# Kernel optimization log

Measured on AMD Instinct MI355X. Metric: run time of the kernel, lower is better.

The kernel has to match this reference:

```python
import jax, jax.numpy as jnp
import numpy as np

N = 200000   # nodes
E = 600000   # edges (avg degree 3, proof graphs are sparse)
L = 4        # num_layers
ND = 64      # ndim (hardcoded in module)
ED = 12      # edim (hardcoded in module)
V = 80       # len(atom_map)
SCALE = 1.0 / np.sqrt(ND).astype(np.float32)


def setup_inputs() -> dict:
    key = jax.random.key(0)
    ks = jax.random.split(key, 20)
    nrm = lambda k, s: jax.random.normal(k, s, jnp.float32) * 0.05
    return {
        "atoms": jax.random.randint(ks[0], (N,), 0, V),
        "edge_index": jax.random.randint(ks[1], (2, E), 0, N),
        "edge_ids": jax.random.randint(ks[2], (E,), 0, 3),
        "atom_emb": nrm(ks[3], (V, ND)),
        "edge_emb": nrm(ks[4], (3, ED)),
        # dim 0: 0 = r2c convs, 1 = c2r convs; dim 1: layer
        "Wq": nrm(ks[5], (2, L, ND, ND)), "bq": nrm(ks[6], (2, L, ND)),
        "Wk": nrm(ks[7], (2, L, ND, ND)), "bk": nrm(ks[8], (2, L, ND)),
        "Wv": nrm(ks[9], (2, L, ND, ND)), "bv": nrm(ks[10], (2, L, ND)),
        "We": nrm(ks[11], (2, L, ED, ND)),            # lin_edge, bias=False (PyG)
        "Ws": nrm(ks[12], (2, L, ND, ND)), "bs": nrm(ks[13], (2, L, ND)),  # root skip
        "aggr_W": nrm(ks[14], (2 * ND, ND)), "aggr_b": nrm(ks[15], (ND,)),
    }


def tconv(x, src, tgt, e_proj, Wq, bq, Wk, bk, Wv, bv, Ws, bs):
    """PyG TransformerConv (heads=1, concat=True, root_weight=True).
    Messages flow src -> tgt; softmax grouped by tgt."""
    q = x @ Wq + bq                                   # [N, ND]
    k = x @ Wk + bk
    v = x @ Wv + bv
    ke = k[src] + e_proj                              # [E, ND]
    ve = v[src] + e_proj
    alpha = jnp.einsum('ed,ed->e', q[tgt], ke) * SCALE
    amax = jax.ops.segment_max(alpha, tgt, num_segments=N)
    ex = jnp.exp(alpha - amax[tgt])
    den = jax.ops.segment_sum(ex, tgt, num_segments=N)
    w = ex / (den[tgt] + 1e-16)                       # segment softmax
    out = jax.ops.segment_sum(ve * w[:, None], tgt, num_segments=N)
    return out + x @ Ws + bs                          # skip connection


def reference(atoms, edge_index, edge_ids, atom_emb, edge_emb,
              Wq, bq, Wk, bk, Wv, bv, We, Ws, bs, aggr_W, aggr_b):
    # dropout omitted (eval mode / identity)
    x = atom_emb[atoms]                               # [N, ND]
    e = edge_emb[edge_ids]                            # [E, ED]
    src, tgt = edge_index[0], edge_index[1]
    for hop in range(L):
        r2c = tconv(x, src, tgt, e @ We[0, hop],
                    Wq[0, hop], bq[0, hop], Wk[0, hop], bk[0, hop],
                    Wv[0, hop], bv[0, hop], Ws[0, hop], bs[0, hop])
        # edge_index.flip(0): swap src/tgt
        c2r = tconv(x, tgt, src, e @ We[1, hop],
                    Wq[1, hop], bq[1, hop], Wk[1, hop], bk[1, hop],
                    Wv[1, hop], bv[1, hop], Ws[1, hop], bs[1, hop])
        h = jnp.concatenate([r2c, c2r], axis=-1) @ aggr_W + aggr_b
        x = jax.nn.gelu(h, approximate=False)         # torch GELU = exact erf
    return x
```

## Files before the change

kernel.cpp:

```cpp
#include <hip/hip_runtime.h>
#include <hip/hip_bf16.h>

typedef unsigned short u16;
typedef unsigned int u32;
typedef unsigned long long u64;
typedef __attribute__((ext_vector_type(8))) short short8v;
typedef __attribute__((ext_vector_type(4))) float f32x4;

#define SCALE 0.125f

__device__ __forceinline__ float bf2f(u16 u){
    union { u32 i; float f; } c; c.i = ((u32)u) << 16; return c.f;
}
__device__ __forceinline__ u16 f2bf(float f){
    __hip_bfloat16 h = __float2bfloat16(f);
    union { __hip_bfloat16 h; u16 u; } c; c.h = h; return c.u;
}

__global__ void k_gather(const int* __restrict__ atoms, const float* __restrict__ emb,
                         float* __restrict__ x, int n){
    int i = blockIdx.x * blockDim.x + threadIdx.x;
    if (i >= n * 16) return;
    int node = i >> 4, f = i & 15;
    int a = atoms[node];
    ((float4*)x)[i] = ((const float4*)emb)[a * 16 + f];
}

__global__ void k_ew(const float* __restrict__ edge_emb, const float* __restrict__ We,
                     float* __restrict__ EW){
    int t = blockIdx.x * blockDim.x + threadIdx.x;
    if (t >= 2 * 4 * 3 * 64) return;
    int j = t & 63, r = t >> 6;
    int eid = r % 3, dh = r / 3;
    float s = 0.f;
    for (int c = 0; c < 12; ++c)
        s += edge_emb[eid * 12 + c] * We[(dh * 12 + c) * 64 + j];
    EW[(dh * 3 + eid) * 64 + j] = s;
}

__global__ void k_count(const int* __restrict__ ei, u32* cnt_t, u32* cnt_s, int E){
    int e = blockIdx.x * blockDim.x + threadIdx.x;
    if (e >= E) return;
    atomicAdd(&cnt_t[ei[E + e]], 1u);
    atomicAdd(&cnt_s[ei[e]], 1u);
}

__global__ __launch_bounds__(256) void k_scan(
    const u32* __restrict__ cnt_t, const u32* __restrict__ cnt_s,
    u32* __restrict__ start_t, u32* __restrict__ start_s,
    u64* __restrict__ totals, int n)
{
    __shared__ u32 wsum_t[4], wsum_s[4];
    __shared__ u32 base_t, base_s;
    const int t0 = blockIdx.x * 1024 + threadIdx.x * 4;
    u32 ct[4], cs[4];
    #pragma unroll
    for (int j = 0; j < 4; ++j){
        int idx = t0 + j;
        ct[j] = (idx < n) ? cnt_t[idx] : 0u;
        cs[j] = (idx < n) ? cnt_s[idx] : 0u;
    }
    u32 tsum_t = ct[0] + ct[1] + ct[2] + ct[3];
    u32 tsum_s = cs[0] + cs[1] + cs[2] + cs[3];
    const int lane = threadIdx.x & 63, wv = threadIdx.x >> 6;
    u32 it = tsum_t, is = tsum_s;
    for (int d = 1; d < 64; d <<= 1){
        u32 a = __shfl_up(it, d);
        u32 b = __shfl_up(is, d);
        if (lane >= d){ it += a; is += b; }
    }
    if (lane == 63){ wsum_t[wv] = it; wsum_s[wv] = is; }
    __syncthreads();
    if (threadIdx.x == 0){
        u32 a0 = wsum_t[0], a1 = wsum_t[1], a2 = wsum_t[2], a3 = wsum_t[3];
        u32 b0 = wsum_s[0], b1 = wsum_s[1], b2 = wsum_s[2], b3 = wsum_s[3];
        u64 old = atomicAdd(totals, ((u64)(b0 + b1 + b2 + b3) << 32) | (u64)(a0 + a1 + a2 + a3));
        base_t = (u32)(old & 0xFFFFFFFFull);
        base_s = (u32)(old >> 32);
        wsum_t[0] = 0; wsum_t[1] = a0; wsum_t[2] = a0 + a1; wsum_t[3] = a0 + a1 + a2;
        wsum_s[0] = 0; wsum_s[1] = b0; wsum_s[2] = b0 + b1; wsum_s[3] = b0 + b1 + b2;
    }
    __syncthreads();
    u32 ex_t = base_t + wsum_t[wv] + (it - tsum_t);
    u32 ex_s = base_s + wsum_s[wv] + (is - tsum_s);
    #pragma unroll
    for (int j = 0; j < 4; ++j){
        int idx = t0 + j;
        if (idx < n){
            start_t[idx] = ex_t; start_s[idx] = ex_s;
            ex_t += ct[j]; ex_s += cs[j];
        }
    }
}

__global__ void k_fill(const int* __restrict__ ei, const int* __restrict__ eids,
                       const u32* __restrict__ start_t, const u32* __restrict__ start_s,
                       u32* cur_t, u32* cur_s, int* adj_t, int* adj_s, int E){
    int e = blockIdx.x * blockDim.x + threadIdx.x;
    if (e >= E) return;
    int s = ei[e], t = ei[E + e], id = eids[e];
    u32 p = atomicAdd(&cur_t[t], 1u);
    adj_t[start_t[t] + p] = s | (id << 20);
    u32 p2 = atomicAdd(&cur_s[s], 1u);
    adj_s[start_s[s] + p2] = t | (id << 20);
}

__global__ __launch_bounds__(256) void k_gemm4(
    const float* __restrict__ x,
    const float* __restrict__ Wq, const float* __restrict__ bq,
    const float* __restrict__ Wk, const float* __restrict__ bk,
    const float* __restrict__ Wv, const float* __restrict__ bv,
    const float* __restrict__ Ws, const float* __restrict__ bs,
    int dh,
    u16* __restrict__ q, u16* __restrict__ k, u16* __restrict__ v,
    float* __restrict__ outd, int n)
{
    __shared__ __align__(16) u16 Wt[4][64][64];
    __shared__ __align__(16) u16 Xh[64][64];
    __shared__ __align__(16) u16 Xl[64][64];
    const int tid = threadIdx.x;
    const int row0 = blockIdx.x * 64;

    const float* wsrc[4] = { Wq + dh * 4096, Wk + dh * 4096, Wv + dh * 4096, Ws + dh * 4096 };
    for (int m = 0; m < 4; ++m){
        for (int i = tid; i < 1024; i += 256){
            int kk = i >> 4, n4 = (i & 15) * 4;
            float4 w = ((const float4*)(wsrc[m] + (size_t)kk * 64))[i & 15];
            float wf[4] = { w.x, w.y, w.z, w.w };
            #pragma unroll
            for (int c = 0; c < 4; ++c){
                int nn = n4 + c;
                int ps = (kk >> 3) ^ (nn & 7);
                Wt[m][nn][ps * 8 + (kk & 7)] = f2bf(wf[c]);
            }
        }
    }
    for (int i = tid; i < 1024; i += 256){
        int r = i >> 4, f = i & 15;
        int gr = row0 + r;
        float4 val = {0.f,0.f,0.f,0.f};
        if (gr < n) val = ((const float4*)x)[(size_t)gr * 16 + f];
        float fv[4] = { val.x, val.y, val.z, val.w };
        int ps = (f >> 1) ^ (r & 7);
        int base = ps * 8 + (f & 1) * 4;
        #pragma unroll
        for (int c = 0; c < 4; ++c){
            u16 hb = f2bf(fv[c]);
            Xh[r][base + c] = hb;
            Xl[r][base + c] = f2bf(fv[c] - bf2f(hb));
        }
    }
    __syncthreads();

    const int wv = tid >> 6, l = tid & 63;
    const int lr = l & 15, lk = l >> 4;
    short8v ah[2], al[2];
    #pragma unroll
    for (int ks = 0; ks < 2; ++ks){
        int r = wv * 16 + lr;
        int ps = (lk + 4 * ks) ^ (r & 7);
        ah[ks] = *(const short8v*)&Xh[r][ps * 8];
        al[ks] = *(const short8v*)&Xl[r][ps * 8];
    }
    const float* bsrc[4] = { bq + dh * 64, bk + dh * 64, bv + dh * 64, bs + dh * 64 };
    u16* outs[3] = { q, k, v };
    for (int m = 0; m < 4; ++m){
        #pragma unroll
        for (int ct = 0; ct < 4; ++ct){
            int col = ct * 16 + lr;
            int s0 = (lk + 0) ^ (col & 7);
            int s1 = (lk + 4) ^ (col & 7);
            short8v b0 = *(const short8v*)&Wt[m][col][s0 * 8];
            short8v b1 = *(const short8v*)&Wt[m][col][s1 * 8];
            float bb = bsrc[m][col];
            f32x4 acc = { bb, bb, bb, bb };
            acc = __builtin_amdgcn_mfma_f32_16x16x32_bf16(ah[0], b0, acc, 0, 0, 0);
            acc = __builtin_amdgcn_mfma_f32_16x16x32_bf16(al[0], b0, acc, 0, 0, 0);
            acc = __builtin_amdgcn_mfma_f32_16x16x32_bf16(ah[1], b1, acc, 0, 0, 0);
            acc = __builtin_amdgcn_mfma_f32_16x16x32_bf16(al[1], b1, acc, 0, 0, 0);
            int grb = row0 + wv * 16 + lk * 4;
            if (m < 3){
                u16* o = outs[m];
                #pragma unroll
                for (int j = 0; j < 4; ++j)
                    if (grb + j < n) o[(size_t)(grb + j) * 64 + col] = f2bf(acc[j]);
            } else {
                #pragma unroll
                for (int j = 0; j < 4; ++j)
                    if (grb + j < n) outd[(size_t)(grb + j) * 64 + col] = acc[j];
            }
        }
    }
}

__global__ __launch_bounds__(256) void k_attn(
    const u16* __restrict__ q, const u16* __restrict__ k, const u16* __restrict__ v,
    const int* __restrict__ adj, const u32* __restrict__ start, const u32* __restrict__ cnt,
    const float* __restrict__ EW, float* __restrict__ outd, int n)
{
    int tid = blockIdx.x * blockDim.x + threadIdx.x;
    int node = tid >> 4;
    int l = tid & 15;
    if (node >= n) return;
    int st = (int)start[node];
    int c  = (int)cnt[node];
    ushort4 qu = ((const ushort4*)q)[node * 16 + l];
    float qx = bf2f(qu.x), qy = bf2f(qu.y), qz = bf2f(qu.z), qw = bf2f(qu.w);
    float4 acc = {0.f, 0.f, 0.f, 0.f};
    float s = 0.f;
    for (int i = 0; i < c; ++i){
        int a = adj[st + i];
        int srcn = a & 0xFFFFF;
        int eid  = ((u32)a) >> 20;
        float4 ew = ((const float4*)EW)[eid * 16 + l];
        ushort4 ku = ((const ushort4*)k)[srcn * 16 + l];
        float kx = bf2f(ku.x) + ew.x, ky = bf2f(ku.y) + ew.y;
        float kz = bf2f(ku.z) + ew.z, kw = bf2f(ku.w) + ew.w;
        float d = qx * kx + qy * ky + qz * kz + qw * kw;
        d += __shfl_xor(d, 1); d += __shfl_xor(d, 2);
        d += __shfl_xor(d, 4); d += __shfl_xor(d, 8);
        float ex = expf(d * SCALE);
        ushort4 vu = ((const ushort4*)v)[srcn * 16 + l];
        acc.x += ex * (bf2f(vu.x) + ew.x);
        acc.y += ex * (bf2f(vu.y) + ew.y);
        acc.z += ex * (bf2f(vu.z) + ew.z);
        acc.w += ex * (bf2f(vu.w) + ew.w);
        s += ex;
    }
    float inv = 1.0f / (s + 1e-16f);
    float4 o = ((float4*)outd)[node * 16 + l];
    o.x += acc.x * inv; o.y += acc.y * inv; o.z += acc.z * inv; o.w += acc.w * inv;
    ((float4*)outd)[node * 16 + l] = o;
}

__global__ __launch_bounds__(256) void k_aggr(
    const float* __restrict__ o0, const float* __restrict__ o1,
    const float* __restrict__ A, const float* __restrict__ b,
    float* __restrict__ x, float* __restrict__ out_f, int write_out, int n)
{
    __shared__ __align__(16) u16 Wt[64][128];
    __shared__ __align__(16) u16 Ah[64][128];
    __shared__ __align__(16) u16 Al_[64][128];
    const int tid = threadIdx.x;
    const int row0 = blockIdx.x * 64;

    for (int i = tid; i < 2048; i += 256){
        int kk = i >> 4, n4 = (i & 15) * 4;
        float4 w = ((const float4*)(A + (size_t)kk * 64))[i & 15];
        float wf[4] = { w.x, w.y, w.z, w.w };
        #pragma unroll
        for (int c = 0; c < 4; ++c){
            int nn = n4 + c;
            int ps = (kk >> 3) ^ (nn & 7);
            Wt[nn][ps * 8 + (kk & 7)] = f2bf(wf[c]);
        }
    }
    for (int i = tid; i < 2048; i += 256){
        int r = i >> 5, f = i & 31;
        int gr = row0 + r;
        float4 val = {0.f,0.f,0.f,0.f};
        if (gr < n){
            if (f < 16) val = ((const float4*)o0)[(size_t)gr * 16 + f];
            else        val = ((const float4*)o1)[(size_t)gr * 16 + (f - 16)];
        }
        float fv[4] = { val.x, val.y, val.z, val.w };
        int ps = (f >> 1) ^ (r & 7);
        int base = ps * 8 + (f & 1) * 4;
        #pragma unroll
        for (int c = 0; c < 4; ++c){
            u16 hb = f2bf(fv[c]);
            Ah[r][base + c] = hb;
            Al_[r][base + c] = f2bf(fv[c] - bf2f(hb));
        }
    }
    __syncthreads();

    const int wv = tid >> 6, l = tid & 63;
    const int lr = l & 15, lk = l >> 4;
    short8v ah[4], al[4];
    #pragma unroll
    for (int ks = 0; ks < 4; ++ks){
        int r = wv * 16 + lr;
        int ps = (lk + 4 * ks) ^ (r & 7);
        ah[ks] = *(const short8v*)&Ah[r][ps * 8];
        al[ks] = *(const short8v*)&Al_[r][ps * 8];
    }
    #pragma unroll
    for (int ct = 0; ct < 4; ++ct){
        int col = ct * 16 + lr;
        float bb = b[col];
        f32x4 acc = { bb, bb, bb, bb };
        #pragma unroll
        for (int ks = 0; ks < 4; ++ks){
            int ps = (lk + 4 * ks) ^ (col & 7);
            short8v bf = *(const short8v*)&Wt[col][ps * 8];
            acc = __builtin_amdgcn_mfma_f32_16x16x32_bf16(ah[ks], bf, acc, 0, 0, 0);
            acc = __builtin_amdgcn_mfma_f32_16x16x32_bf16(al[ks], bf, acc, 0, 0, 0);
        }
        int grb = row0 + wv * 16 + lk * 4;
        #pragma unroll
        for (int j = 0; j < 4; ++j){
            if (grb + j >= n) continue;
            float h = acc[j];
            float g = 0.5f * h * (1.0f + erff(h * 0.70710678118654752f));
            x[(size_t)(grb + j) * 64 + col] = g;
            if (write_out) out_f[(size_t)(grb + j) * 64 + col] = g;
        }
    }
}

extern "C" void kernel_launch(void* const* d_in, const int* in_sizes, int n_in,
                              void* d_out, int out_size, void* d_ws, size_t ws_size,
                              hipStream_t stream)
{
    const int* atoms      = (const int*)d_in[0];
    const int* ei         = (const int*)d_in[1];
    const int* eids       = (const int*)d_in[2];
    const float* atom_emb = (const float*)d_in[3];
    const float* edge_emb = (const float*)d_in[4];
    const float* Wq = (const float*)d_in[5];  const float* bq = (const float*)d_in[6];
    const float* Wk = (const float*)d_in[7];  const float* bk = (const float*)d_in[8];
    const float* Wv = (const float*)d_in[9];  const float* bv = (const float*)d_in[10];
    const float* We = (const float*)d_in[11];
    const float* Ws = (const float*)d_in[12]; const float* bs = (const float*)d_in[13];
    const float* aggr_W = (const float*)d_in[14];
    const float* aggr_b = (const float*)d_in[15];

    const int N = in_sizes[0];
    const int E = in_sizes[1] / 2;

    char* p = (char*)d_ws;
    auto alloc = [&](size_t bytes){
        void* r = (void*)p;
        p += (bytes + 255) & ~(size_t)255;
        return r;
    };
    float* x   = (float*)alloc((size_t)N * 64 * 4);
    u16*   qb  = (u16*)  alloc((size_t)N * 64 * 2);
    u16*   kb  = (u16*)  alloc((size_t)N * 64 * 2);
    u16*   vb  = (u16*)  alloc((size_t)N * 64 * 2);
    float* o0  = (float*)alloc((size_t)N * 64 * 4);
    float* o1  = (float*)alloc((size_t)N * 64 * 4);
    float* EWt = (float*)alloc(2 * 4 * 3 * 64 * 4);
    int* adj_t = (int*)alloc((size_t)E * 4);
    int* adj_s = (int*)alloc((size_t)E * 4);
    u32* start_t = (u32*)alloc((size_t)N * 4);
    u32* start_s = (u32*)alloc((size_t)N * 4);
    u32* zb = (u32*)alloc(((size_t)4 * N + 2) * 4);
    u32* cnt_t = zb;
    u32* cnt_s = zb + N;
    u32* cur_t = zb + 2 * (size_t)N;
    u32* cur_s = zb + 3 * (size_t)N;
    u64* totals = (u64*)(zb + 4 * (size_t)N);

    hipMemsetAsync(zb, 0, ((size_t)4 * N + 2) * 4, stream);

    k_gather<<<(N * 16 + 255) / 256, 256, 0, stream>>>(atoms, atom_emb, x, N);
    k_ew<<<6, 256, 0, stream>>>(edge_emb, We, EWt);
    k_count<<<(E + 255) / 256, 256, 0, stream>>>(ei, cnt_t, cnt_s, E);
    k_scan<<<(N + 1023) / 1024, 256, 0, stream>>>(cnt_t, cnt_s, start_t, start_s, totals, N);
    k_fill<<<(E + 255) / 256, 256, 0, stream>>>(ei, eids, start_t, start_s, cur_t, cur_s, adj_t, adj_s, E);

    const int gB = (N + 63) / 64;
    const int gA = (N * 16 + 255) / 256;
    for (int hop = 0; hop < 4; ++hop){
        int dh0 = hop;
        int dh1 = 4 + hop;
        k_gemm4<<<gB, 256, 0, stream>>>(x, Wq, bq, Wk, bk, Wv, bv, Ws, bs, dh0, qb, kb, vb, o0, N);
        k_attn<<<gA, 256, 0, stream>>>(qb, kb, vb, adj_t, start_t, cnt_t, EWt + dh0 * 192, o0, N);
        k_gemm4<<<gB, 256, 0, stream>>>(x, Wq, bq, Wk, bk, Wv, bv, Ws, bs, dh1, qb, kb, vb, o1, N);
        k_attn<<<gA, 256, 0, stream>>>(qb, kb, vb, adj_s, start_s, cnt_s, EWt + dh1 * 192, o1, N);
        k_aggr<<<gB, 256, 0, stream>>>(o0, o1, aggr_W, aggr_b, x, (float*)d_out, hop == 3 ? 1 : 0, N);
    }
}
```

Before: 1.382 ms.

## Store node features and conv outputs in bf16, drop split-bf16 GEMM passes

Switches the node feature buffer x and the per-direction conv outputs o0/o1 from fp32 to bf16 storage. The GEMM kernels now load bf16 directly into LDS and drop the hi/lo split-precision MFMA passes, halving MFMA count. Memory traffic for x, o0 and o1 is halved in the gather, GEMM, attention and aggregation kernels. The cost is lower accuracy: activations and skip/attention accumulations are rounded to bf16 at every layer.

```diff
diff --git a/kernel.cpp b/kernel.cpp
--- a/kernel.cpp
+++ b/kernel.cpp
@@ -18,12 +18,14 @@
 }
 
 __global__ void k_gather(const int* __restrict__ atoms, const float* __restrict__ emb,
-                         float* __restrict__ x, int n){
+                         u16* __restrict__ x, int n){
     int i = blockIdx.x * blockDim.x + threadIdx.x;
     if (i >= n * 16) return;
     int node = i >> 4, f = i & 15;
     int a = atoms[node];
-    ((float4*)x)[i] = ((const float4*)emb)[a * 16 + f];
+    float4 v = ((const float4*)emb)[a * 16 + f];
+    ushort4 o = { f2bf(v.x), f2bf(v.y), f2bf(v.z), f2bf(v.w) };
+    ((ushort4*)x)[i] = o;
 }
 
 __global__ void k_ew(const float* __restrict__ edge_emb, const float* __restrict__ We,
@@ -106,18 +108,17 @@
 }
 
 __global__ __launch_bounds__(256) void k_gemm4(
-    const float* __restrict__ x,
+    const u16* __restrict__ x,
     const float* __restrict__ Wq, const float* __restrict__ bq,
     const float* __restrict__ Wk, const float* __restrict__ bk,
     const float* __restrict__ Wv, const float* __restrict__ bv,
     const float* __restrict__ Ws, const float* __restrict__ bs,
     int dh,
     u16* __restrict__ q, u16* __restrict__ k, u16* __restrict__ v,
-    float* __restrict__ outd, int n)
+    u16* __restrict__ outd, int n)
 {
     __shared__ __align__(16) u16 Wt[4][64][64];
     __shared__ __align__(16) u16 Xh[64][64];
-    __shared__ __align__(16) u16 Xl[64][64];
     const int tid = threadIdx.x;
     const int row0 = blockIdx.x * 64;
 
@@ -135,35 +136,27 @@
             }
         }
     }
-    for (int i = tid; i < 1024; i += 256){
-        int r = i >> 4, f = i & 15;
+    for (int i = tid; i < 512; i += 256){
+        int r = i >> 3, f = i & 7;
         int gr = row0 + r;
-        float4 val = {0.f,0.f,0.f,0.f};
-        if (gr < n) val = ((const float4*)x)[(size_t)gr * 16 + f];
-        float fv[4] = { val.x, val.y, val.z, val.w };
-        int ps = (f >> 1) ^ (r & 7);
-        int base = ps * 8 + (f & 1) * 4;
-        #pragma unroll
-        for (int c = 0; c < 4; ++c){
-            u16 hb = f2bf(fv[c]);
-            Xh[r][base + c] = hb;
-            Xl[r][base + c] = f2bf(fv[c] - bf2f(hb));
-        }
+        short8v val = {0,0,0,0,0,0,0,0};
+        if (gr < n) val = *(const short8v*)&x[(size_t)gr * 64 + f * 8];
+        int ps = f ^ (r & 7);
+        *(short8v*)&Xh[r][ps * 8] = val;
     }
     __syncthreads();
 
     const int wv = tid >> 6, l = tid & 63;
     const int lr = l & 15, lk = l >> 4;
-    short8v ah[2], al[2];
+    short8v ah[2];
     #pragma unroll
     for (int ks = 0; ks < 2; ++ks){
         int r = wv * 16 + lr;
         int ps = (lk + 4 * ks) ^ (r & 7);
         ah[ks] = *(const short8v*)&Xh[r][ps * 8];
-        al[ks] = *(const short8v*)&Xl[r][ps * 8];
     }
     const float* bsrc[4] = { bq + dh * 64, bk + dh * 64, bv + dh * 64, bs + dh * 64 };
-    u16* outs[3] = { q, k, v };
+    u16* outs[4] = { q, k, v, outd };
     for (int m = 0; m < 4; ++m){
         #pragma unroll
         for (int ct = 0; ct < 4; ++ct){
@@ -175,20 +168,12 @@
             float bb = bsrc[m][col];
             f32x4 acc = { bb, bb, bb, bb };
             acc = __builtin_amdgcn_mfma_f32_16x16x32_bf16(ah[0], b0, acc, 0, 0, 0);
-            acc = __builtin_amdgcn_mfma_f32_16x16x32_bf16(al[0], b0, acc, 0, 0, 0);
             acc = __builtin_amdgcn_mfma_f32_16x16x32_bf16(ah[1], b1, acc, 0, 0, 0);
-            acc = __builtin_amdgcn_mfma_f32_16x16x32_bf16(al[1], b1, acc, 0, 0, 0);
             int grb = row0 + wv * 16 + lk * 4;
-            if (m < 3){
-                u16* o = outs[m];
-                #pragma unroll
-                for (int j = 0; j < 4; ++j)
-                    if (grb + j < n) o[(size_t)(grb + j) * 64 + col] = f2bf(acc[j]);
-            } else {
-                #pragma unroll
-                for (int j = 0; j < 4; ++j)
-                    if (grb + j < n) outd[(size_t)(grb + j) * 64 + col] = acc[j];
-            }
+            u16* o = outs[m];
+            #pragma unroll
+            for (int j = 0; j < 4; ++j)
+                if (grb + j < n) o[(size_t)(grb + j) * 64 + col] = f2bf(acc[j]);
         }
     }
 }
@@ -196,7 +181,7 @@
 __global__ __launch_bounds__(256) void k_attn(
     const u16* __restrict__ q, const u16* __restrict__ k, const u16* __restrict__ v,
     const int* __restrict__ adj, const u32* __restrict__ start, const u32* __restrict__ cnt,
-    const float* __restrict__ EW, float* __restrict__ outd, int n)
+    const float* __restrict__ EW, u16* __restrict__ outd, int n)
 {
     int tid = blockIdx.x * blockDim.x + threadIdx.x;
     int node = tid >> 4;
@@ -228,19 +213,19 @@
         s += ex;
     }
     float inv = 1.0f / (s + 1e-16f);
-    float4 o = ((float4*)outd)[node * 16 + l];
-    o.x += acc.x * inv; o.y += acc.y * inv; o.z += acc.z * inv; o.w += acc.w * inv;
-    ((float4*)outd)[node * 16 + l] = o;
+    ushort4 ou = ((const ushort4*)outd)[node * 16 + l];
+    ushort4 no = { f2bf(bf2f(ou.x) + acc.x * inv), f2bf(bf2f(ou.y) + acc.y * inv),
+                   f2bf(bf2f(ou.z) + acc.z * inv), f2bf(bf2f(ou.w) + acc.w * inv) };
+    ((ushort4*)outd)[node * 16 + l] = no;
 }
 
 __global__ __launch_bounds__(256) void k_aggr(
-    const float* __restrict__ o0, const float* __restrict__ o1,
+    const u16* __restrict__ o0, const u16* __restrict__ o1,
     const float* __restrict__ A, const float* __restrict__ b,
-    float* __restrict__ x, float* __restrict__ out_f, int write_out, int n)
+    u16* __restrict__ x, float* __restrict__ out_f, int write_out, int n)
 {
     __shared__ __align__(16) u16 Wt[64][128];
     __shared__ __align__(16) u16 Ah[64][128];
-    __shared__ __align__(16) u16 Al_[64][128];
     const int tid = threadIdx.x;
     const int row0 = blockIdx.x * 64;
 
@@ -255,35 +240,27 @@
             Wt[nn][ps * 8 + (kk & 7)] = f2bf(wf[c]);
         }
     }
-    for (int i = tid; i < 2048; i += 256){
-        int r = i >> 5, f = i & 31;
+    for (int i = tid; i < 1024; i += 256){
+        int r = i >> 4, j = i & 15;
         int gr = row0 + r;
-        float4 val = {0.f,0.f,0.f,0.f};
+        short8v val = {0,0,0,0,0,0,0,0};
         if (gr < n){
-            if (f < 16) val = ((const float4*)o0)[(size_t)gr * 16 + f];
-            else        val = ((const float4*)o1)[(size_t)gr * 16 + (f - 16)];
-        }
-        float fv[4] = { val.x, val.y, val.z, val.w };
-        int ps = (f >> 1) ^ (r & 7);
-        int base = ps * 8 + (f & 1) * 4;
-        #pragma unroll
-        for (int c = 0; c < 4; ++c){
-            u16 hb = f2bf(fv[c]);
-            Ah[r][base + c] = hb;
-            Al_[r][base + c] = f2bf(fv[c] - bf2f(hb));
-        }
+            if (j < 8) val = *(const short8v*)&o0[(size_t)gr * 64 + j * 8];
+            else       val = *(const short8v*)&o1[(size_t)gr * 64 + (j - 8) * 8];
+        }
+        int ps = j ^ (r & 7);
+        *(short8v*)&Ah[r][ps * 8] = val;
     }
     __syncthreads();
 
     const int wv = tid >> 6, l = tid & 63;
     const int lr = l & 15, lk = l >> 4;
-    short8v ah[4], al[4];
+    short8v ah[4];
     #pragma unroll
     for (int ks = 0; ks < 4; ++ks){
         int r = wv * 16 + lr;
         int ps = (lk + 4 * ks) ^ (r & 7);
         ah[ks] = *(const short8v*)&Ah[r][ps * 8];
-        al[ks] = *(const short8v*)&Al_[r][ps * 8];
     }
     #pragma unroll
     for (int ct = 0; ct < 4; ++ct){
@@ -295,7 +272,6 @@
             int ps = (lk + 4 * ks) ^ (col & 7);
             short8v bf = *(const short8v*)&Wt[col][ps * 8];
             acc = __builtin_amdgcn_mfma_f32_16x16x32_bf16(ah[ks], bf, acc, 0, 0, 0);
-            acc = __builtin_amdgcn_mfma_f32_16x16x32_bf16(al[ks], bf, acc, 0, 0, 0);
         }
         int grb = row0 + wv * 16 + lk * 4;
         #pragma unroll
@@ -303,7 +279,7 @@
             if (grb + j >= n) continue;
             float h = acc[j];
             float g = 0.5f * h * (1.0f + erff(h * 0.70710678118654752f));
-            x[(size_t)(grb + j) * 64 + col] = g;
+            x[(size_t)(grb + j) * 64 + col] = f2bf(g);
             if (write_out) out_f[(size_t)(grb + j) * 64 + col] = g;
         }
     }
@@ -335,12 +311,12 @@
         p += (bytes + 255) & ~(size_t)255;
         return r;
     };
-    float* x   = (float*)alloc((size_t)N * 64 * 4);
+    u16*   x   = (u16*)  alloc((size_t)N * 64 * 2);
     u16*   qb  = (u16*)  alloc((size_t)N * 64 * 2);
     u16*   kb  = (u16*)  alloc((size_t)N * 64 * 2);
     u16*   vb  = (u16*)  alloc((size_t)N * 64 * 2);
-    float* o0  = (float*)alloc((size_t)N * 64 * 4);
-    float* o1  = (float*)alloc((size_t)N * 64 * 4);
+    u16*   o0  = (u16*)  alloc((size_t)N * 64 * 2);
+    u16*   o1  = (u16*)  alloc((size_t)N * 64 * 2);
     float* EWt = (float*)alloc(2 * 4 * 3 * 64 * 4);
     int* adj_t = (int*)alloc((size_t)E * 4);
     int* adj_s = (int*)alloc((size_t)E * 4);
```

Result: faster. 1.122 ms (-18.8%).
